# Performance work log

Hardware: AMD Instinct MI355X
Metric: run time of the kernel (lower is better)

Reference implementation:

```python
import jax, jax.numpy as jnp
import numpy as np

GRID_SIZE = 5
SPLINE_ORDER = 3
KH, KW = 3, 3
STRIDE, PAD, DIL = 1, 1, 1


def make_grid(in_features, dtype=jnp.float32):
    # uniform grid over [-1, 1], extended by spline_order on each side
    h = 2.0 / GRID_SIZE
    g = jnp.arange(-SPLINE_ORDER, GRID_SIZE + SPLINE_ORDER + 1, dtype=dtype) * h - 1.0
    return jnp.broadcast_to(g, (in_features, g.shape[0]))  # (in, G)


def b_splines(x, grid):
    # x: (N, in); grid: (in, G). Cox-de Boor recursion.
    xg = x[..., None]  # (N, in, 1)
    bases = ((xg >= grid[:, :-1]) & (xg < grid[:, 1:])).astype(x.dtype)  # (N, in, G-1)
    for k in range(1, SPLINE_ORDER + 1):
        left = (xg - grid[:, : -(k + 1)]) / (grid[:, k:-1] - grid[:, : -(k + 1)])
        right = (grid[:, k + 1:] - xg) / (grid[:, k + 1:] - grid[:, 1:-k])
        bases = left * bases[..., :-1] + right * bases[..., 1:]
    return bases  # (N, in, grid_size + spline_order)


def setup_inputs() -> dict:
    key = jax.random.key(0)
    k1, k2, k3, k4 = jax.random.split(key, 4)
    B, C, H, W = 4, 64, 64, 64
    out_ch = 128
    patch_dim = C * KH * KW  # 576
    nbasis = GRID_SIZE + SPLINE_ORDER  # 8
    x = jax.random.normal(k1, (B, C, H, W), dtype=jnp.float32)
    base_weight = jax.random.normal(k2, (out_ch, patch_dim), dtype=jnp.float32) * 0.05
    spline_weight = jax.random.normal(k3, (out_ch, patch_dim, nbasis), dtype=jnp.float32) * 0.05
    spline_scaler = jax.random.normal(k4, (out_ch, patch_dim), dtype=jnp.float32) * 0.1 + 1.0
    return {"x": x, "base_weight": base_weight, "spline_weight": spline_weight, "spline_scaler": spline_scaler}


def reference(x, base_weight, spline_weight, spline_scaler):
    B, C, H, W = x.shape
    out_ch, patch_dim = base_weight.shape
    # im2col: (B, C*KH*KW, Ho, Wo), feature dim ordered (C, kh, kw) like F.unfold
    patches = jax.lax.conv_general_dilated_patches(
        x, filter_shape=(KH, KW), window_strides=(STRIDE, STRIDE),
        padding=((PAD, PAD), (PAD, PAD)), rhs_dilation=(DIL, DIL),
        dimension_numbers=("NCHW", "OIHW", "NCHW"))
    Ho = (H + 2 * PAD - DIL * (KH - 1) - 1) // STRIDE + 1
    Wo = (W + 2 * PAD - DIL * (KW - 1) - 1) // STRIDE + 1
    L = Ho * Wo
    p = patches.reshape(B, patch_dim, L).transpose(0, 2, 1).reshape(B * L, patch_dim)  # (N, D)
    grid = make_grid(patch_dim, p.dtype)
    base_out = jax.nn.silu(p) @ base_weight.T  # (N, out)
    bases = b_splines(p, grid)  # (N, D, nbasis)
    scaled_w = spline_weight * spline_scaler[..., None]  # (out, D, nbasis)
    spline_out = jnp.einsum("ndk,odk->no", bases, scaled_w)
    out = (base_out + spline_out).reshape(B, L, out_ch).transpose(0, 2, 1).reshape(B, out_ch, Ho, Wo)
    return out
```

## Files before the change

### kernel.cpp

```cpp
#include <hip/hip_runtime.h>
#include <hip/hip_bf16.h>

#define B_      4
#define C_IN    64
#define H_      64
#define W_      64
#define OUT_CH  128
#define HP_     66
#define CF      576
#define WP_BYTES  (9 * OUT_CH * CF * 2)
#define F_BYTES   (B_ * HP_ * HP_ * CF * 2)
#define P_OFFSET  (WP_BYTES + F_BYTES)

typedef __bf16 bf16x8 __attribute__((ext_vector_type(8)));
typedef float  f32x4  __attribute__((ext_vector_type(4)));
typedef _Float16 half8 __attribute__((ext_vector_type(8)));

__device__ __forceinline__ void compute_features(float x, float f[9]) {
    f[0] = x / (1.0f + __expf(-x));
    float g[12];
#pragma unroll
    for (int i = 0; i < 12; ++i) g[i] = (float)(i - 3) * 0.4f - 1.0f;
    float bb[11];
#pragma unroll
    for (int i = 0; i < 11; ++i) bb[i] = (x >= g[i] && x < g[i + 1]) ? 1.0f : 0.0f;
#pragma unroll
    for (int i = 0; i < 10; ++i)
        bb[i] = (x - g[i]) * (1.0f / (g[i + 1] - g[i])) * bb[i]
              + (g[i + 2] - x) * (1.0f / (g[i + 2] - g[i + 1])) * bb[i + 1];
#pragma unroll
    for (int i = 0; i < 9; ++i)
        bb[i] = (x - g[i]) * (1.0f / (g[i + 2] - g[i])) * bb[i]
              + (g[i + 3] - x) * (1.0f / (g[i + 3] - g[i + 1])) * bb[i + 1];
#pragma unroll
    for (int i = 0; i < 8; ++i)
        bb[i] = (x - g[i]) * (1.0f / (g[i + 3] - g[i])) * bb[i]
              + (g[i + 4] - x) * (1.0f / (g[i + 4] - g[i + 1])) * bb[i + 1];
#pragma unroll
    for (int i = 0; i < 8; ++i) f[1 + i] = bb[i];
}

__global__ __launch_bounds__(256) void pack_kernel(
        const float* __restrict__ bw, const float* __restrict__ sw,
        const float* __restrict__ sc, __hip_bfloat16* __restrict__ Wp) {
    int idx = blockIdx.x * 256 + threadIdx.x;
    if (idx < 589824) {
        int o = idx / 4608;
        int r = idx - o * 4608;
        int d = r >> 3;
        int j = r & 7;
        int tap = d % 9;
        int c   = d / 9;
        float v = sw[idx] * sc[o * 576 + d];
        Wp[(tap * OUT_CH + o) * CF + (j + 1) * 64 + c] = __float2bfloat16(v);
    } else {
        int k = idx - 589824;
        int o = k / 576;
        int d = k - o * 576;
        int tap = d % 9;
        int c   = d / 9;
        Wp[(tap * OUT_CH + o) * CF + c] = __float2bfloat16(bw[k]);
    }
}

__global__ __launch_bounds__(256) void feat_kernel(
        const float* __restrict__ x, __hip_bfloat16* __restrict__ F) {
    __shared__ float xs[64][65];
    int b  = blockIdx.x / HP_;
    int hp = blockIdx.x % HP_;
    int h  = hp - 1;
    int tid = threadIdx.x;

    float f0[9];
    compute_features(0.0f, f0);

    bool interior_row = (h >= 0) && (h < H_);
    if (interior_row) {
        int wl  = tid & 63;
        int c16 = tid >> 6;
#pragma unroll
        for (int i = 0; i < 16; ++i) {
            int c = c16 * 16 + i;
            xs[c][wl] = x[((b * C_IN + c) * H_ + h) * W_ + wl];
        }
    }
    __syncthreads();

    int c  = tid & 63;
    int wg = tid >> 6;
    __hip_bfloat16* Frow = F + (size_t)((b * HP_ + hp) * HP_) * CF;

    if (!interior_row) {
        for (int wp = wg; wp < HP_; wp += 4) {
            __hip_bfloat16* dst = Frow + (size_t)wp * CF + c;
#pragma unroll
            for (int j = 0; j < 9; ++j) dst[j * 64] = __float2bfloat16(f0[j]);
        }
        return;
    }
    if (wg == 0) {
        __hip_bfloat16* dst = Frow + c;
#pragma unroll
        for (int j = 0; j < 9; ++j) dst[j * 64] = __float2bfloat16(f0[j]);
    }
    if (wg == 3) {
        __hip_bfloat16* dst = Frow + (size_t)65 * CF + c;
#pragma unroll
        for (int j = 0; j < 9; ++j) dst[j * 64] = __float2bfloat16(f0[j]);
    }
    for (int w2 = wg; w2 < 64; w2 += 4) {
        float xv = xs[c][w2];
        float f[9];
        compute_features(xv, f);
        __hip_bfloat16* dst = Frow + (size_t)(w2 + 1) * CF + c;
#pragma unroll
        for (int j = 0; j < 9; ++j) dst[j * 64] = __float2bfloat16(f[j]);
    }
}

__global__ __launch_bounds__(256, 2) void gemm_kernel(
        const __hip_bfloat16* __restrict__ Fb, const __hip_bfloat16* __restrict__ Wpb,
        _Float16* __restrict__ P) {
    __shared__ __align__(16) ushort As[2][8192];
    __shared__ __align__(16) ushort Bs[2][8192];

    const ushort* F  = (const ushort*)Fb;
    const ushort* Wp = (const ushort*)Wpb;

    int tid  = threadIdx.x;
    int lane = tid & 63;
    int w    = tid >> 6;
    int l15  = lane & 15;
    int lq   = lane >> 4;
    int wm = w & 1;
    int wn = w >> 1;
    int srow = lane >> 3;
    int sl7  = lane & 7;
    int c8s  = sl7 ^ srow;

    int blk = blockIdx.x;
    int g   = blk >> 7;
    int t   = blk & 127;
    int b   = t >> 5;
    int ho0 = (t & 31) << 1;
    int c0 = (g == 0) ? 0 : (21 + 20 * (g - 1));
    int c1 = c0 + ((g == 0) ? 21 : 20);

    f32x4 acc[4][4];
#pragma unroll
    for (int i = 0; i < 4; ++i)
#pragma unroll
        for (int j = 0; j < 4; ++j) acc[i][j] = (f32x4){0.f, 0.f, 0.f, 0.f};

    auto prefetch = [&](int ch, int buf) {
        int tap = ch / 9;
        int kc  = ch - tap * 9;
        int kh  = tap / 3;
        int kw  = tap - kh * 3;
#pragma unroll
        for (int r = 0; r < 4; ++r) {
            int row = (r * 4 + w) * 8 + srow;
            int hp = ho0 + (row >> 6) + kh;
            int wp = (row & 63) + kw;
            const ushort* srcA = F + (size_t)((b * HP_ + hp) * HP_ + wp) * CF
                                   + kc * 64 + c8s * 8;
            __builtin_amdgcn_global_load_lds(
                (const __attribute__((address_space(1))) unsigned int*)srcA,
                (__attribute__((address_space(3))) unsigned int*)&As[buf][(r * 4 + w) * 512],
                16, 0, 0);
            const ushort* srcB = Wp + (size_t)(tap * OUT_CH + row) * CF
                                    + kc * 64 + c8s * 8;
            __builtin_amdgcn_global_load_lds(
                (const __attribute__((address_space(1))) unsigned int*)srcB,
                (__attribute__((address_space(3))) unsigned int*)&Bs[buf][(r * 4 + w) * 512],
                16, 0, 0);
        }
    };

    int buf = 0;
    prefetch(c0, 0);
    for (int ch = c0; ch < c1; ++ch) {
        __syncthreads();
        if (ch + 1 < c1) prefetch(ch + 1, buf ^ 1);
#pragma unroll
        for (int ks = 0; ks < 2; ++ks) {
            bf16x8 af[4], bq[4];
#pragma unroll
            for (int mt = 0; mt < 4; ++mt) {
                int o  = wm * 64 + mt * 16 + l15;
                int sl = o * 8 + ((ks * 4 + lq) ^ (o & 7));
                af[mt] = *(const bf16x8*)&Bs[buf][sl * 8];
            }
#pragma unroll
            for (int nt = 0; nt < 4; ++nt) {
                int p  = wn * 64 + nt * 16 + l15;
                int sl = p * 8 + ((ks * 4 + lq) ^ (p & 7));
                bq[nt] = *(const bf16x8*)&As[buf][sl * 8];
            }
#pragma unroll
            for (int mt = 0; mt < 4; ++mt)
#pragma unroll
                for (int nt = 0; nt < 4; ++nt)
                    acc[mt][nt] = __builtin_amdgcn_mfma_f32_16x16x32_bf16(
                        af[mt], bq[nt], acc[mt][nt], 0, 0, 0);
        }
        buf ^= 1;
    }

    _Float16* Pg = P + ((size_t)(g * 4 + b) * OUT_CH) * 4096 + ho0 * 64;
#pragma unroll
    for (int mt = 0; mt < 4; ++mt) {
        int o = wm * 64 + mt * 16 + lq * 4;
#pragma unroll
        for (int nt = 0; nt < 4; ++nt) {
            int pix = wn * 64 + nt * 16 + l15;
            _Float16* dst = Pg + (size_t)o * 4096 + pix;
#pragma unroll
            for (int r = 0; r < 4; ++r)
                dst[(size_t)r * 4096] = (_Float16)acc[mt][nt][r];
        }
    }
}

__global__ __launch_bounds__(256) void reduce_kernel(
        const half8* __restrict__ P, float4* __restrict__ out) {
    const int GS = 262144;
    int i = blockIdx.x * 256 + threadIdx.x;
    half8 a = P[i], bb = P[GS + i], c = P[2 * GS + i], d = P[3 * GS + i];
    float4 o0, o1;
#pragma unroll
    for (int j = 0; j < 4; ++j)
        ((float*)&o0)[j] = (float)a[j] + (float)bb[j] + (float)c[j] + (float)d[j];
#pragma unroll
    for (int j = 0; j < 4; ++j)
        ((float*)&o1)[j] = (float)a[4 + j] + (float)bb[4 + j] + (float)c[4 + j] + (float)d[4 + j];
    out[i * 2]     = o0;
    out[i * 2 + 1] = o1;
}

extern "C" void kernel_launch(void* const* d_in, const int* in_sizes, int n_in,
                              void* d_out, int out_size, void* d_ws, size_t ws_size,
                              hipStream_t stream) {
    const float* x  = (const float*)d_in[0];
    const float* bw = (const float*)d_in[1];
    const float* sw = (const float*)d_in[2];
    const float* sc = (const float*)d_in[3];
    float* out = (float*)d_out;

    __hip_bfloat16* Wp = (__hip_bfloat16*)d_ws;
    __hip_bfloat16* F  = (__hip_bfloat16*)((char*)d_ws + WP_BYTES);
    _Float16*       P  = (_Float16*)((char*)d_ws + P_OFFSET);

    pack_kernel<<<2592, 256, 0, stream>>>(bw, sw, sc, Wp);
    feat_kernel<<<B_ * HP_, 256, 0, stream>>>(x, F);
    gemm_kernel<<<512, 256, 0, stream>>>(F, Wp, P);
    reduce_kernel<<<1024, 256, 0, stream>>>((const half8*)P, (float4*)out);
}
```

Measured before the change: 116.0 us.

## Reuse staged feature rows across all 3x3 taps in implicit GEMM

The GEMM now stages a 4-row by 68-column halo tile of the padded feature map once per 32-channel slice. It reads all nine taps from that shared-memory tile by shifting the pixel index, instead of reloading im2col rows for every tap. The weight slice per tap becomes smaller and is double-buffered per tap. The K split grows to 6 groups (768 blocks, occupancy hint 3), and the reduce kernel sums 6 partials. This cuts global and L2 traffic for activations, at the cost of more barriers per K and extra partial-sum traffic in the reduce.

```diff
diff --git a/kernel.cpp b/kernel.cpp
--- a/kernel.cpp
+++ b/kernel.cpp
@@ -11,6 +11,7 @@
 #define WP_BYTES  (9 * OUT_CH * CF * 2)
 #define F_BYTES   (B_ * HP_ * HP_ * CF * 2)
 #define P_OFFSET  (WP_BYTES + F_BYTES)
+#define NSPLIT  6
 
 typedef __bf16 bf16x8 __attribute__((ext_vector_type(8)));
 typedef float  f32x4  __attribute__((ext_vector_type(4)));
@@ -118,11 +119,11 @@
     }
 }
 
-__global__ __launch_bounds__(256, 2) void gemm_kernel(
+__global__ __launch_bounds__(256, 3) void gemm_kernel(
         const __hip_bfloat16* __restrict__ Fb, const __hip_bfloat16* __restrict__ Wpb,
         _Float16* __restrict__ P) {
-    __shared__ __align__(16) ushort As[2][8192];
-    __shared__ __align__(16) ushort Bs[2][8192];
+    __shared__ __align__(16) ushort Fs[2][1088 * 8];
+    __shared__ __align__(16) ushort Bs[2][512 * 8];
 
     const ushort* F  = (const ushort*)Fb;
     const ushort* Wp = (const ushort*)Wpb;
@@ -132,19 +133,15 @@
     int w    = tid >> 6;
     int l15  = lane & 15;
     int lq   = lane >> 4;
-    int wm = w & 1;
-    int wn = w >> 1;
-    int srow = lane >> 3;
-    int sl7  = lane & 7;
-    int c8s  = sl7 ^ srow;
+    int wm   = w & 1;
+    int wn   = w >> 1;
 
     int blk = blockIdx.x;
-    int g   = blk >> 7;
+    int ug  = blk >> 7;
     int t   = blk & 127;
     int b   = t >> 5;
     int ho0 = (t & 31) << 1;
-    int c0 = (g == 0) ? 0 : (21 + 20 * (g - 1));
-    int c1 = c0 + ((g == 0) ? 21 : 20);
+    int u0  = ug * 3;
 
     f32x4 acc[4][4];
 #pragma unroll
@@ -152,50 +149,78 @@
 #pragma unroll
         for (int j = 0; j < 4; ++j) acc[i][j] = (f32x4){0.f, 0.f, 0.f, 0.f};
 
-    auto prefetch = [&](int ch, int buf) {
-        int tap = ch / 9;
-        int kc  = ch - tap * 9;
-        int kh  = tap / 3;
-        int kw  = tap - kh * 3;
-#pragma unroll
-        for (int r = 0; r < 4; ++r) {
-            int row = (r * 4 + w) * 8 + srow;
-            int hp = ho0 + (row >> 6) + kh;
-            int wp = (row & 63) + kw;
-            const ushort* srcA = F + (size_t)((b * HP_ + hp) * HP_ + wp) * CF
-                                   + kc * 64 + c8s * 8;
+    auto stage_b = [&](int u, int tap, int buf) {
+        int kc  = u >> 1;
+        int h32 = u & 1;
+        const ushort* base = Wp + (size_t)(tap * OUT_CH) * CF + kc * 64 + h32 * 32;
+#pragma unroll
+        for (int i = 0; i < 2; ++i) {
+            int sb   = (w * 2 + i) * 64;
+            int slot = sb + lane;
+            int o  = slot >> 2;
+            int c4 = (slot & 3) ^ ((o >> 1) & 3);
+            const ushort* src = base + (size_t)o * CF + c4 * 8;
             __builtin_amdgcn_global_load_lds(
-                (const __attribute__((address_space(1))) unsigned int*)srcA,
-                (__attribute__((address_space(3))) unsigned int*)&As[buf][(r * 4 + w) * 512],
+                (const __attribute__((address_space(1))) unsigned int*)src,
+                (__attribute__((address_space(3))) unsigned int*)&Bs[buf][sb * 8],
                 16, 0, 0);
-            const ushort* srcB = Wp + (size_t)(tap * OUT_CH + row) * CF
-                                    + kc * 64 + c8s * 8;
+        }
+    };
+
+    auto stage_fp = [&](int u, int buf) {
+        int kc  = u >> 1;
+        int h32 = u & 1;
+        const ushort* base = F + (size_t)((b * HP_ + ho0) * HP_) * CF + kc * 64 + h32 * 32;
+#pragma unroll
+        for (int i = 0; i < 5; ++i) {
+            int ch = w + 4 * i;
+            if (ch >= 17) break;
+            int sb   = ch * 64;
+            int slot = sb + lane;
+            int q   = slot >> 2;
+            int row = q / 68;
+            int wp  = q - row * 68;
+            if (wp > 65) wp = 65;
+            int c4 = (slot & 3) ^ ((wp >> 1) & 3);
+            const ushort* src = base + ((size_t)row * HP_ + wp) * CF + c4 * 8;
             __builtin_amdgcn_global_load_lds(
-                (const __attribute__((address_space(1))) unsigned int*)srcB,
-                (__attribute__((address_space(3))) unsigned int*)&Bs[buf][(r * 4 + w) * 512],
+                (const __attribute__((address_space(1))) unsigned int*)src,
+                (__attribute__((address_space(3))) unsigned int*)&Fs[buf][sb * 8],
                 16, 0, 0);
         }
     };
 
-    int buf = 0;
-    prefetch(c0, 0);
-    for (int ch = c0; ch < c1; ++ch) {
-        __syncthreads();
-        if (ch + 1 < c1) prefetch(ch + 1, buf ^ 1);
-#pragma unroll
-        for (int ks = 0; ks < 2; ++ks) {
+    stage_fp(u0, 0);
+    stage_b(u0, 0, 0);
+    int fpb = 0, bb = 0;
+
+    for (int uu = 0; uu < 3; ++uu) {
+        int u = u0 + uu;
+#pragma unroll
+        for (int tap = 0; tap < 9; ++tap) {
+            int kh = tap / 3;
+            int kw = tap - kh * 3;
+            __syncthreads();
+            if (tap < 8) {
+                stage_b(u, tap + 1, bb ^ 1);
+            } else if (uu < 2) {
+                stage_b(u + 1, 0, bb ^ 1);
+                stage_fp(u + 1, fpb ^ 1);
+            }
             bf16x8 af[4], bq[4];
 #pragma unroll
             for (int mt = 0; mt < 4; ++mt) {
-                int o  = wm * 64 + mt * 16 + l15;
-                int sl = o * 8 + ((ks * 4 + lq) ^ (o & 7));
-                af[mt] = *(const bf16x8*)&Bs[buf][sl * 8];
+                int o    = wm * 64 + mt * 16 + l15;
+                int slot = o * 4 + (lq ^ ((o >> 1) & 3));
+                af[mt] = *(const bf16x8*)&Bs[bb][slot * 8];
             }
 #pragma unroll
             for (int nt = 0; nt < 4; ++nt) {
-                int p  = wn * 64 + nt * 16 + l15;
-                int sl = p * 8 + ((ks * 4 + lq) ^ (p & 7));
-                bq[nt] = *(const bf16x8*)&As[buf][sl * 8];
+                int p    = wn * 64 + nt * 16 + l15;
+                int fr   = (p >> 6) + kh;
+                int wp   = (p & 63) + kw;
+                int slot = (fr * 68 + wp) * 4 + (lq ^ ((wp >> 1) & 3));
+                bq[nt] = *(const bf16x8*)&Fs[fpb][slot * 8];
             }
 #pragma unroll
             for (int mt = 0; mt < 4; ++mt)
@@ -203,14 +228,15 @@
                 for (int nt = 0; nt < 4; ++nt)
                     acc[mt][nt] = __builtin_amdgcn_mfma_f32_16x16x32_bf16(
                         af[mt], bq[nt], acc[mt][nt], 0, 0, 0);
-        }
-        buf ^= 1;
-    }
-
-    _Float16* Pg = P + ((size_t)(g * 4 + b) * OUT_CH) * 4096 + ho0 * 64;
+            bb ^= 1;
+        }
+        fpb ^= 1;
+    }
+
+    _Float16* Pg = P + ((size_t)(ug * 4 + b) * OUT_CH) * 4096 + ho0 * 64;
 #pragma unroll
     for (int mt = 0; mt < 4; ++mt) {
-        int o = wm * 64 + mt * 16 + lq * 4;
+        int o = wm * 64 + mt * 16 + (lane >> 4) * 4;
 #pragma unroll
         for (int nt = 0; nt < 4; ++nt) {
             int pix = wn * 64 + nt * 16 + l15;
@@ -226,14 +252,18 @@
         const half8* __restrict__ P, float4* __restrict__ out) {
     const int GS = 262144;
     int i = blockIdx.x * 256 + threadIdx.x;
-    half8 a = P[i], bb = P[GS + i], c = P[2 * GS + i], d = P[3 * GS + i];
+    half8 s[NSPLIT];
+#pragma unroll
+    for (int g = 0; g < NSPLIT; ++g) s[g] = P[g * GS + i];
     float4 o0, o1;
 #pragma unroll
-    for (int j = 0; j < 4; ++j)
-        ((float*)&o0)[j] = (float)a[j] + (float)bb[j] + (float)c[j] + (float)d[j];
-#pragma unroll
-    for (int j = 0; j < 4; ++j)
-        ((float*)&o1)[j] = (float)a[4 + j] + (float)bb[4 + j] + (float)c[4 + j] + (float)d[4 + j];
+    for (int j = 0; j < 4; ++j) {
+        float a = 0.f, bsum = 0.f;
+#pragma unroll
+        for (int g = 0; g < NSPLIT; ++g) { a += (float)s[g][j]; bsum += (float)s[g][4 + j]; }
+        ((float*)&o0)[j] = a;
+        ((float*)&o1)[j] = bsum;
+    }
     out[i * 2]     = o0;
     out[i * 2 + 1] = o1;
 }
@@ -253,6 +283,6 @@
 
     pack_kernel<<<2592, 256, 0, stream>>>(bw, sw, sc, Wp);
     feat_kernel<<<B_ * HP_, 256, 0, stream>>>(x, F);
-    gemm_kernel<<<512, 256, 0, stream>>>(F, Wp, P);
+    gemm_kernel<<<768, 256, 0, stream>>>(F, Wp, P);
     reduce_kernel<<<1024, 256, 0, stream>>>((const half8*)P, (float4*)out);
 }
```

Result: slower. 130.6 us (+12.6%).

## Drop LDS staging in GEMM, load fragments directly, split K six ways

Applied to the files above, without the earlier changes.

The GEMM no longer stages A and B tiles through double-buffered LDS with global_load_lds. Each lane now loads its MFMA fragments straight from global memory, which removes the LDS traffic and the barriers. The K range is split across 6 groups instead of 4, giving 768 blocks at an occupancy hint of 3 blocks per CU. Partials are stored in fragment-native order and the reduce kernel does the scatter into NCHW. This relies on L2 and cache reuse instead of LDS, which risks redundant global loads and exposed latency with no software prefetch. The reduce step also has more partial data to read.

```diff
diff --git a/kernel.cpp b/kernel.cpp
--- a/kernel.cpp
+++ b/kernel.cpp
@@ -11,10 +11,11 @@
 #define WP_BYTES  (9 * OUT_CH * CF * 2)
 #define F_BYTES   (B_ * HP_ * HP_ * CF * 2)
 #define P_OFFSET  (WP_BYTES + F_BYTES)
+#define NSPLIT  6
 
 typedef __bf16 bf16x8 __attribute__((ext_vector_type(8)));
 typedef float  f32x4  __attribute__((ext_vector_type(4)));
-typedef _Float16 half8 __attribute__((ext_vector_type(8)));
+typedef _Float16 half4 __attribute__((ext_vector_type(4)));
 
 __device__ __forceinline__ void compute_features(float x, float f[9]) {
     f[0] = x / (1.0f + __expf(-x));
@@ -118,12 +119,9 @@
     }
 }
 
-__global__ __launch_bounds__(256, 2) void gemm_kernel(
+__global__ __launch_bounds__(256, 3) void gemm_kernel(
         const __hip_bfloat16* __restrict__ Fb, const __hip_bfloat16* __restrict__ Wpb,
-        _Float16* __restrict__ P) {
-    __shared__ __align__(16) ushort As[2][8192];
-    __shared__ __align__(16) ushort Bs[2][8192];
-
+        half4* __restrict__ P) {
     const ushort* F  = (const ushort*)Fb;
     const ushort* Wp = (const ushort*)Wpb;
 
@@ -132,19 +130,16 @@
     int w    = tid >> 6;
     int l15  = lane & 15;
     int lq   = lane >> 4;
-    int wm = w & 1;
-    int wn = w >> 1;
-    int srow = lane >> 3;
-    int sl7  = lane & 7;
-    int c8s  = sl7 ^ srow;
+    int wm   = w & 1;
+    int wn   = w >> 1;
 
     int blk = blockIdx.x;
     int g   = blk >> 7;
     int t   = blk & 127;
     int b   = t >> 5;
     int ho0 = (t & 31) << 1;
-    int c0 = (g == 0) ? 0 : (21 + 20 * (g - 1));
-    int c1 = c0 + ((g == 0) ? 21 : 20);
+    int u0  = (g < 3) ? g * 13 : 39 + (g - 3) * 14;
+    int nu  = (g < 3) ? 13 : 14;
 
     f32x4 acc[4][4];
 #pragma unroll
@@ -152,90 +147,78 @@
 #pragma unroll
         for (int j = 0; j < 4; ++j) acc[i][j] = (f32x4){0.f, 0.f, 0.f, 0.f};
 
-    auto prefetch = [&](int ch, int buf) {
-        int tap = ch / 9;
-        int kc  = ch - tap * 9;
+    const ushort* Wl = Wp + (size_t)(wm * 64 + l15) * CF + lq * 8;
+    const ushort* Fl = F + (size_t)((b * HP_ + ho0 + wn) * HP_ + l15) * CF + lq * 8;
+
+    for (int ui = 0; ui < nu; ++ui) {
+        int u   = u0 + ui;
+        int tap = u / 9;
+        int kc  = u - tap * 9;
         int kh  = tap / 3;
         int kw  = tap - kh * 3;
-#pragma unroll
-        for (int r = 0; r < 4; ++r) {
-            int row = (r * 4 + w) * 8 + srow;
-            int hp = ho0 + (row >> 6) + kh;
-            int wp = (row & 63) + kw;
-            const ushort* srcA = F + (size_t)((b * HP_ + hp) * HP_ + wp) * CF
-                                   + kc * 64 + c8s * 8;
-            __builtin_amdgcn_global_load_lds(
-                (const __attribute__((address_space(1))) unsigned int*)srcA,
-                (__attribute__((address_space(3))) unsigned int*)&As[buf][(r * 4 + w) * 512],
-                16, 0, 0);
-            const ushort* srcB = Wp + (size_t)(tap * OUT_CH + row) * CF
-                                    + kc * 64 + c8s * 8;
-            __builtin_amdgcn_global_load_lds(
-                (const __attribute__((address_space(1))) unsigned int*)srcB,
-                (__attribute__((address_space(3))) unsigned int*)&Bs[buf][(r * 4 + w) * 512],
-                16, 0, 0);
-        }
-    };
-
-    int buf = 0;
-    prefetch(c0, 0);
-    for (int ch = c0; ch < c1; ++ch) {
-        __syncthreads();
-        if (ch + 1 < c1) prefetch(ch + 1, buf ^ 1);
-#pragma unroll
-        for (int ks = 0; ks < 2; ++ks) {
-            bf16x8 af[4], bq[4];
-#pragma unroll
-            for (int mt = 0; mt < 4; ++mt) {
-                int o  = wm * 64 + mt * 16 + l15;
-                int sl = o * 8 + ((ks * 4 + lq) ^ (o & 7));
-                af[mt] = *(const bf16x8*)&Bs[buf][sl * 8];
-            }
-#pragma unroll
-            for (int nt = 0; nt < 4; ++nt) {
-                int p  = wn * 64 + nt * 16 + l15;
-                int sl = p * 8 + ((ks * 4 + lq) ^ (p & 7));
-                bq[nt] = *(const bf16x8*)&As[buf][sl * 8];
-            }
+        int koff = kc * 64;
+        const ushort* wbase = Wl + (size_t)(tap * OUT_CH) * CF + koff;
+        const ushort* fbase = Fl + (size_t)(kh * HP_ + kw) * CF + koff;
+
+        bf16x8 af[4][2], bf[4][2];
+#pragma unroll
+        for (int ks = 0; ks < 2; ++ks)
+#pragma unroll
+            for (int mt = 0; mt < 4; ++mt)
+                af[mt][ks] = *(const bf16x8*)(wbase + (size_t)mt * 16 * CF + ks * 32);
+#pragma unroll
+        for (int ks = 0; ks < 2; ++ks)
+#pragma unroll
+            for (int nt = 0; nt < 4; ++nt)
+                bf[nt][ks] = *(const bf16x8*)(fbase + (size_t)nt * 16 * CF + ks * 32);
+#pragma unroll
+        for (int ks = 0; ks < 2; ++ks)
 #pragma unroll
             for (int mt = 0; mt < 4; ++mt)
 #pragma unroll
                 for (int nt = 0; nt < 4; ++nt)
                     acc[mt][nt] = __builtin_amdgcn_mfma_f32_16x16x32_bf16(
-                        af[mt], bq[nt], acc[mt][nt], 0, 0, 0);
+                        af[mt][ks], bf[nt][ks], acc[mt][nt], 0, 0, 0);
+    }
+
+    half4* Pp = P + ((size_t)blk * 4 + w) * 16 * 64 + lane;
+#pragma unroll
+    for (int mt = 0; mt < 4; ++mt)
+#pragma unroll
+        for (int nt = 0; nt < 4; ++nt) {
+            half4 h;
+#pragma unroll
+            for (int r = 0; r < 4; ++r) h[r] = (_Float16)acc[mt][nt][r];
+            Pp[(mt * 4 + nt) * 64] = h;
         }
-        buf ^= 1;
-    }
-
-    _Float16* Pg = P + ((size_t)(g * 4 + b) * OUT_CH) * 4096 + ho0 * 64;
-#pragma unroll
-    for (int mt = 0; mt < 4; ++mt) {
-        int o = wm * 64 + mt * 16 + lq * 4;
-#pragma unroll
-        for (int nt = 0; nt < 4; ++nt) {
-            int pix = wn * 64 + nt * 16 + l15;
-            _Float16* dst = Pg + (size_t)o * 4096 + pix;
-#pragma unroll
-            for (int r = 0; r < 4; ++r)
-                dst[(size_t)r * 4096] = (_Float16)acc[mt][nt][r];
-        }
-    }
 }
 
 __global__ __launch_bounds__(256) void reduce_kernel(
-        const half8* __restrict__ P, float4* __restrict__ out) {
-    const int GS = 262144;
+        const half4* __restrict__ P, float* __restrict__ out) {
+    const int GS = 524288;
     int i = blockIdx.x * 256 + threadIdx.x;
-    half8 a = P[i], bb = P[GS + i], c = P[2 * GS + i], d = P[3 * GS + i];
-    float4 o0, o1;
-#pragma unroll
-    for (int j = 0; j < 4; ++j)
-        ((float*)&o0)[j] = (float)a[j] + (float)bb[j] + (float)c[j] + (float)d[j];
-#pragma unroll
-    for (int j = 0; j < 4; ++j)
-        ((float*)&o1)[j] = (float)a[4 + j] + (float)bb[4 + j] + (float)c[4 + j] + (float)d[4 + j];
-    out[i * 2]     = o0;
-    out[i * 2 + 1] = o1;
+    float s[4] = {0.f, 0.f, 0.f, 0.f};
+#pragma unroll
+    for (int g = 0; g < NSPLIT; ++g) {
+        half4 v = P[(size_t)g * GS + i];
+#pragma unroll
+        for (int r = 0; r < 4; ++r) s[r] += (float)v[r];
+    }
+    int lane = i & 63;
+    int frag = (i >> 6) & 15;
+    int w    = (i >> 10) & 3;
+    int t    = i >> 12;
+    int l15 = lane & 15, lq = lane >> 4;
+    int mt = frag >> 2, nt = frag & 3;
+    int wm = w & 1, wn = w >> 1;
+    int b  = t >> 5;
+    int ho = ((t & 31) << 1) + wn;
+    int o  = wm * 64 + mt * 16 + lq * 4;
+    int wo = nt * 16 + l15;
+    float* dst = out + ((size_t)(b * OUT_CH + o) << 12) + (ho << 6) + wo;
+#pragma unroll
+    for (int r = 0; r < 4; ++r)
+        dst[(size_t)r << 12] = s[r];
 }
 
 extern "C" void kernel_launch(void* const* d_in, const int* in_sizes, int n_in,
@@ -249,10 +232,10 @@
 
     __hip_bfloat16* Wp = (__hip_bfloat16*)d_ws;
     __hip_bfloat16* F  = (__hip_bfloat16*)((char*)d_ws + WP_BYTES);
-    _Float16*       P  = (_Float16*)((char*)d_ws + P_OFFSET);
+    half4*          P  = (half4*)((char*)d_ws + P_OFFSET);
 
     pack_kernel<<<2592, 256, 0, stream>>>(bw, sw, sc, Wp);
     feat_kernel<<<B_ * HP_, 256, 0, stream>>>(x, F);
-    gemm_kernel<<<512, 256, 0, stream>>>(F, Wp, P);
-    reduce_kernel<<<1024, 256, 0, stream>>>((const half8*)P, (float4*)out);
-}
+    gemm_kernel<<<768, 256, 0, stream>>>(F, Wp, P);
+    reduce_kernel<<<2048, 256, 0, stream>>>(P, out);
+}
```

After: 169.7 us. 46.4% more time.

## Triple-buffer A tiles in GEMM and split feature rows across two blocks

Applied to the files above, without the earlier changes.

The GEMM mainloop now keeps three LDS buffers for the activation tile and two for the weight tile. It prefetches A two chunks ahead and waits on explicit vmcnt values instead of a full __syncthreads, so the scattered im2col loads get more time in flight. Separately, the feature kernel launches twice as many blocks, each handling half of a padded row, to raise parallelism. LDS use per GEMM block grows by 16 KB, which may limit occupancy. The hand-coded waitcnt immediates must match the number of outstanding loads exactly, or the pipeline reads stale data.

```diff
diff --git a/kernel.cpp b/kernel.cpp
--- a/kernel.cpp
+++ b/kernel.cpp
@@ -66,10 +66,12 @@
 __global__ __launch_bounds__(256) void feat_kernel(
         const float* __restrict__ x, __hip_bfloat16* __restrict__ F) {
     __shared__ float xs[64][65];
-    int b  = blockIdx.x / HP_;
-    int hp = blockIdx.x % HP_;
-    int h  = hp - 1;
-    int tid = threadIdx.x;
+    int blk  = blockIdx.x;
+    int half = blk & 1;
+    int hp   = (blk >> 1) % HP_;
+    int b    = blk / (2 * HP_);
+    int h    = hp - 1;
+    int tid  = threadIdx.x;
 
     float f0[9];
     compute_features(0.0f, f0);
@@ -91,24 +93,26 @@
     __hip_bfloat16* Frow = F + (size_t)((b * HP_ + hp) * HP_) * CF;
 
     if (!interior_row) {
-        for (int wp = wg; wp < HP_; wp += 4) {
+        int wp0 = half * 33;
+        for (int wp = wp0 + wg; wp < wp0 + 33; wp += 4) {
             __hip_bfloat16* dst = Frow + (size_t)wp * CF + c;
 #pragma unroll
             for (int j = 0; j < 9; ++j) dst[j * 64] = __float2bfloat16(f0[j]);
         }
         return;
     }
-    if (wg == 0) {
+    if (half == 0 && wg == 0) {
         __hip_bfloat16* dst = Frow + c;
 #pragma unroll
         for (int j = 0; j < 9; ++j) dst[j * 64] = __float2bfloat16(f0[j]);
     }
-    if (wg == 3) {
+    if (half == 1 && wg == 3) {
         __hip_bfloat16* dst = Frow + (size_t)65 * CF + c;
 #pragma unroll
         for (int j = 0; j < 9; ++j) dst[j * 64] = __float2bfloat16(f0[j]);
     }
-    for (int w2 = wg; w2 < 64; w2 += 4) {
+    int w2base = half * 32;
+    for (int w2 = w2base + wg; w2 < w2base + 32; w2 += 4) {
         float xv = xs[c][w2];
         float f[9];
         compute_features(xv, f);
@@ -121,7 +125,7 @@
 __global__ __launch_bounds__(256, 2) void gemm_kernel(
         const __hip_bfloat16* __restrict__ Fb, const __hip_bfloat16* __restrict__ Wpb,
         _Float16* __restrict__ P) {
-    __shared__ __align__(16) ushort As[2][8192];
+    __shared__ __align__(16) ushort As[3][8192];
     __shared__ __align__(16) ushort Bs[2][8192];
 
     const ushort* F  = (const ushort*)Fb;
@@ -144,7 +148,7 @@
     int b   = t >> 5;
     int ho0 = (t & 31) << 1;
     int c0 = (g == 0) ? 0 : (21 + 20 * (g - 1));
-    int c1 = c0 + ((g == 0) ? 21 : 20);
+    int n  = (g == 0) ? 21 : 20;
 
     f32x4 acc[4][4];
 #pragma unroll
@@ -152,7 +156,7 @@
 #pragma unroll
         for (int j = 0; j < 4; ++j) acc[i][j] = (f32x4){0.f, 0.f, 0.f, 0.f};
 
-    auto prefetch = [&](int ch, int buf) {
+    auto prefetchA = [&](int ch, int buf) {
         int tap = ch / 9;
         int kc  = ch - tap * 9;
         int kh  = tap / 3;
@@ -168,6 +172,14 @@
                 (const __attribute__((address_space(1))) unsigned int*)srcA,
                 (__attribute__((address_space(3))) unsigned int*)&As[buf][(r * 4 + w) * 512],
                 16, 0, 0);
+        }
+    };
+    auto prefetchB = [&](int ch, int buf) {
+        int tap = ch / 9;
+        int kc  = ch - tap * 9;
+#pragma unroll
+        for (int r = 0; r < 4; ++r) {
+            int row = (r * 4 + w) * 8 + srow;
             const ushort* srcB = Wp + (size_t)(tap * OUT_CH + row) * CF
                                     + kc * 64 + c8s * 8;
             __builtin_amdgcn_global_load_lds(
@@ -177,11 +189,18 @@
         }
     };
 
-    int buf = 0;
-    prefetch(c0, 0);
-    for (int ch = c0; ch < c1; ++ch) {
-        __syncthreads();
-        if (ch + 1 < c1) prefetch(ch + 1, buf ^ 1);
+    prefetchB(c0, 0);
+    prefetchA(c0, 0);
+    if (n > 1) prefetchA(c0 + 1, 1);
+
+    for (int i = 0; i < n; ++i) {
+        if (i + 1 < n) __builtin_amdgcn_s_waitcnt(0xF74);
+        else           __builtin_amdgcn_s_waitcnt(0xF70);
+        __builtin_amdgcn_s_barrier();
+        if (i + 1 < n) prefetchB(c0 + i + 1, (i + 1) & 1);
+        if (i + 2 < n) prefetchA(c0 + i + 2, (i + 2) % 3);
+        const ushort* Ab = As[i % 3];
+        const ushort* Bb = Bs[i & 1];
 #pragma unroll
         for (int ks = 0; ks < 2; ++ks) {
             bf16x8 af[4], bq[4];
@@ -189,13 +208,13 @@
             for (int mt = 0; mt < 4; ++mt) {
                 int o  = wm * 64 + mt * 16 + l15;
                 int sl = o * 8 + ((ks * 4 + lq) ^ (o & 7));
-                af[mt] = *(const bf16x8*)&Bs[buf][sl * 8];
+                af[mt] = *(const bf16x8*)&Bb[sl * 8];
             }
 #pragma unroll
             for (int nt = 0; nt < 4; ++nt) {
                 int p  = wn * 64 + nt * 16 + l15;
                 int sl = p * 8 + ((ks * 4 + lq) ^ (p & 7));
-                bq[nt] = *(const bf16x8*)&As[buf][sl * 8];
+                bq[nt] = *(const bf16x8*)&Ab[sl * 8];
             }
 #pragma unroll
             for (int mt = 0; mt < 4; ++mt)
@@ -204,7 +223,6 @@
                     acc[mt][nt] = __builtin_amdgcn_mfma_f32_16x16x32_bf16(
                         af[mt], bq[nt], acc[mt][nt], 0, 0, 0);
         }
-        buf ^= 1;
     }
 
     _Float16* Pg = P + ((size_t)(g * 4 + b) * OUT_CH) * 4096 + ho0 * 64;
@@ -252,7 +270,7 @@
     _Float16*       P  = (_Float16*)((char*)d_ws + P_OFFSET);
 
     pack_kernel<<<2592, 256, 0, stream>>>(bw, sw, sc, Wp);
-    feat_kernel<<<B_ * HP_, 256, 0, stream>>>(x, F);
+    feat_kernel<<<B_ * HP_ * 2, 256, 0, stream>>>(x, F);
     gemm_kernel<<<512, 256, 0, stream>>>(F, Wp, P);
     reduce_kernel<<<1024, 256, 0, stream>>>((const half8*)P, (float4*)out);
 }
```

After: 119.9 us. +3.4%, slower.
